# Kernel tuning notes

Hardware: AMD Instinct MI355X
Metric: run time of the kernel (lower is better)

Reference implementation:

```python
import jax, jax.numpy as jnp
import numpy as np

DIM = 256
HEAD_DIM = 64
NH = DIM // HEAD_DIM
PS = 2  # fine patch size
EPS = 1e-5


def _conv(x, w, b, stride, pad):
    y = jax.lax.conv_general_dilated(x, w, (stride, stride), ((pad, pad), (pad, pad)),
                                     dimension_numbers=('NCHW', 'OIHW', 'NCHW'))
    return y + b[None, :, None, None]


def _bn(x, g, b, m, v):
    s = g * jax.lax.rsqrt(v + EPS)
    return x * s[None, :, None, None] + (b - m * s)[None, :, None, None]


def setup_inputs() -> dict:
    key = jax.random.key(0)
    ks = jax.random.split(key, 24)
    C = DIM
    d = {}
    d['x'] = jax.random.normal(ks[0], (8, C, 64, 64), jnp.float32)
    # Downsample conv (C->C, k=4, s=2, p=1), torch OIHW layout
    d['w_down'] = jax.random.normal(ks[1], (C, C, 4, 4), jnp.float32) * 0.02
    d['b_down'] = jax.random.normal(ks[2], (C,), jnp.float32) * 0.02
    # coarse to_qkv Linear(64 -> 192), stored as [in, out]
    d['w_qkv_c'] = jax.random.normal(ks[3], (HEAD_DIM, 3 * HEAD_DIM), jnp.float32) * 0.05
    d['b_qkv_c'] = jax.random.normal(ks[4], (3 * HEAD_DIM,), jnp.float32) * 0.02
    # Upsample ConvTranspose2d (torch [in, out, kH, kW] layout)
    d['w_up'] = jax.random.normal(ks[5], (C, C, 4, 4), jnp.float32) * 0.02
    d['b_up'] = jax.random.normal(ks[6], (C,), jnp.float32) * 0.02
    # fine to_qkv Linear(64 -> 192)
    d['w_qkv_f'] = jax.random.normal(ks[7], (HEAD_DIM, 3 * HEAD_DIM), jnp.float32) * 0.05
    d['b_qkv_f'] = jax.random.normal(ks[8], (3 * HEAD_DIM,), jnp.float32) * 0.02
    # DWConv: depthwise 3x3 (groups=C) -> BN -> relu6 -> pointwise 1x1 -> BN -> relu6
    d['w_dw'] = jax.random.normal(ks[9], (C, 1, 3, 3), jnp.float32) * 0.1
    d['bn_dw_g'] = jax.random.uniform(ks[10], (C,), jnp.float32) * 0.5 + 0.75
    d['bn_dw_b'] = jax.random.normal(ks[11], (C,), jnp.float32) * 0.1
    d['bn_dw_m'] = jax.random.normal(ks[12], (C,), jnp.float32) * 0.1
    d['bn_dw_v'] = jax.random.uniform(ks[13], (C,), jnp.float32) + 0.5
    d['w_pw'] = jax.random.normal(ks[14], (C, C, 1, 1), jnp.float32) * 0.05
    d['bn_pw_g'] = jax.random.uniform(ks[15], (C,), jnp.float32) * 0.5 + 0.75
    d['bn_pw_b'] = jax.random.normal(ks[16], (C,), jnp.float32) * 0.1
    d['bn_pw_m'] = jax.random.normal(ks[17], (C,), jnp.float32) * 0.1
    d['bn_pw_v'] = jax.random.uniform(ks[18], (C,), jnp.float32) + 0.5
    return d


def reference(x, w_down, b_down, w_qkv_c, b_qkv_c, w_up, b_up, w_qkv_f, b_qkv_f,
              w_dw, bn_dw_g, bn_dw_b, bn_dw_m, bn_dw_v,
              w_pw, bn_pw_g, bn_pw_b, bn_pw_m, bn_pw_v):
    B, C, H, W = x.shape
    nh, hd = C // HEAD_DIM, HEAD_DIM
    scale = hd ** -0.5

    # ---- CoarseSelfAttention ----
    xd = _conv(x, w_down, b_down, 2, 1)           # [B,C,h,w]
    h, w = xd.shape[2], xd.shape[3]
    P = h * w
    tok = xd.reshape(B, nh, hd, P).transpose(0, 1, 3, 2)   # [B,nh,P,hd]
    q, k, v = jnp.split(tok @ w_qkv_c + b_qkv_c, 3, axis=-1)
    attn = jax.nn.softmax(jnp.einsum('bhqd,bhkd->bhqk', q, k) * scale, axis=-1)
    coarse_score = attn.sum(axis=-2)               # [B,nh,P]
    kf = max(1, P // 4)
    top_k = jax.lax.top_k(coarse_score, kf)[1]     # [B,nh,kf]
    out = jnp.einsum('bhqk,bhkd->bhqd', attn, v)
    out = out.transpose(0, 1, 3, 2).reshape(B, C, h, w)
    # ConvTranspose2d(k=4,s=2,p=1) as lhs-dilated conv with flipped/transposed kernel
    wt = jnp.flip(w_up, (2, 3)).transpose(1, 0, 2, 3)
    coarse = jax.lax.conv_general_dilated(out, wt, (1, 1), ((2, 2), (2, 2)),
                                          lhs_dilation=(2, 2),
                                          dimension_numbers=('NCHW', 'OIHW', 'NCHW'))
    coarse = coarse + b_up[None, :, None, None]
    # F.interpolate to (H,W) is identity here: upsample exactly restores HxW

    # ---- TopkSelfAttention ----
    ph, pw = H // PS, W // PS                      # ph*pw == P
    xh = coarse.reshape(B, nh, hd, ph, PS, pw, PS)
    patches = xh.transpose(0, 1, 2, 3, 5, 4, 6).reshape(B, nh, hd, ph * pw, PS, PS)
    idx = jnp.broadcast_to(top_k[:, :, None, :, None, None], (B, nh, hd, kf, PS, PS))
    sel = jnp.take_along_axis(patches, idx, axis=3)        # [B,nh,hd,kf,PS,PS]
    tokf = sel.reshape(B, nh, hd, kf, PS * PS).transpose(0, 1, 3, 4, 2)
    tokf = tokf.reshape(B, nh, kf * PS * PS, hd)
    qf, kk, vf = jnp.split(tokf @ w_qkv_f + b_qkv_f, 3, axis=-1)
    attnf = jax.nn.softmax(jnp.einsum('bhqd,bhkd->bhqk', qf, kk) * scale, axis=-1)
    outf = jnp.einsum('bhqk,bhkd->bhqd', attnf, vf)
    outf = outf.reshape(B, nh, kf, PS * PS, hd).transpose(0, 1, 2, 4, 3)
    outf = outf.reshape(B, nh, kf, hd, PS, PS)     # [B,nh,kf,hd,PS,PS]
    # scatter selected patches back into zeros (topk indices are unique per b,h)
    res = jnp.zeros((B, nh, ph * pw, hd, PS, PS), x.dtype)
    bi = jnp.arange(B)[:, None, None]
    hi = jnp.arange(nh)[None, :, None]
    res = res.at[bi, hi, top_k].set(outf)
    res = res.transpose(0, 1, 3, 2, 4, 5).reshape(B, nh, hd, ph, pw, PS, PS)
    region = res.transpose(0, 1, 2, 3, 5, 4, 6).reshape(B, C, H, W)

    y = coarse + region

    # ---- DWConv feed-forward ----
    yd = jax.lax.conv_general_dilated(y, w_dw, (1, 1), ((1, 1), (1, 1)),
                                      feature_group_count=C,
                                      dimension_numbers=('NCHW', 'OIHW', 'NCHW'))
    yd = jnp.clip(_bn(yd, bn_dw_g, bn_dw_b, bn_dw_m, bn_dw_v), 0.0, 6.0)
    yp = jax.lax.conv_general_dilated(yd, w_pw, (1, 1), ((0, 0), (0, 0)),
                                      dimension_numbers=('NCHW', 'OIHW', 'NCHW'))
    yp = jnp.clip(_bn(yp, bn_pw_g, bn_pw_b, bn_pw_m, bn_pw_v), 0.0, 6.0)
    return yp
```

## Files before the change

### kernel.cpp

```cpp
#include <hip/hip_runtime.h>
#include <cstdint>
#include <cstddef>


#define EPS_ 1e-5f

typedef short bf16x8_t __attribute__((ext_vector_type(8)));
typedef float f32x4_t __attribute__((ext_vector_type(4)));
#define MFMA16(a, b, c) __builtin_amdgcn_mfma_f32_16x16x32_bf16(a, b, c, 0, 0, 0)

__device__ __forceinline__ void cvt1(float f, unsigned short& h, unsigned short& l) {
  unsigned u = __float_as_uint(f);
  unsigned r = u + 0x7FFFu + ((u >> 16) & 1u);
  h = (unsigned short)(r >> 16);
  float lo = f - __uint_as_float(r & 0xFFFF0000u);
  l = (unsigned short)(__float_as_uint(lo) >> 16);
}
__device__ __forceinline__ void cvt2(float f0, float f1, unsigned& hpack, unsigned& lpack) {
  unsigned u0 = __float_as_uint(f0), u1 = __float_as_uint(f1);
  unsigned r0 = u0 + 0x7FFFu + ((u0 >> 16) & 1u);
  unsigned r1 = u1 + 0x7FFFu + ((u1 >> 16) & 1u);
  hpack = (r0 >> 16) | (r1 & 0xFFFF0000u);
  float l0 = f0 - __uint_as_float(r0 & 0xFFFF0000u);
  float l1 = f1 - __uint_as_float(r1 & 0xFFFF0000u);
  lpack = (__float_as_uint(l0) >> 16) | (__float_as_uint(l1) & 0xFFFF0000u);
}

__global__ __launch_bounds__(256) void k_pad_x(
    const float* __restrict__ x, float* __restrict__ xp) {
  const int plane = blockIdx.x;
  const float* src = x + (size_t)plane * 4096;
  float* dst = xp + (size_t)plane * 4356;
  for (int e = threadIdx.x; e < 4356; e += 256) {
    int r = e / 66, cc = e - r * 66;
    float v = 0.f;
    if (r >= 1 && r <= 64 && cc >= 1 && cc <= 64) v = src[(r - 1) * 64 + (cc - 1)];
    dst[e] = v;
  }
}

__global__ __launch_bounds__(256) void k_cvt_wdown(
    const float* __restrict__ w, unsigned short* __restrict__ wh,
    unsigned short* __restrict__ wl) {
  int e = blockIdx.x * 256 + threadIdx.x;
  cvt1(w[e], wh[e], wl[e]);
}

__global__ __launch_bounds__(256) void k_cvt_wqkv(
    const float* __restrict__ wq, unsigned short* __restrict__ wh,
    unsigned short* __restrict__ wl) {
  int e = blockIdx.x * 256 + threadIdx.x;
  int col = e >> 6, d = e & 63;
  float f = wq[d * 192 + col];
  if (col < 64) f *= 0.125f;
  cvt1(f, wh[e], wl[e]);
}

__global__ __launch_bounds__(256) void k_cvt_wup(
    const float* __restrict__ w_up, unsigned short* __restrict__ wth,
    unsigned short* __restrict__ wtl) {
  int e = blockIdx.x * 256 + threadIdx.x;
  int kp = e & 1023, oc = (e >> 10) & 255, c = e >> 18;
  int tap = kp >> 8, ic = kp & 255;
  int tk = tap >> 1, txi = tap & 1;
  int ry = c >> 1, rx = c & 1;
  int ky = (1 - ry) + 2 * tk, kx = (1 - rx) + 2 * txi;
  cvt1(w_up[((size_t)(ic * 256 + oc) * 4 + ky) * 4 + kx], wth[e], wtl[e]);
}

__global__ __launch_bounds__(256) void k_cvt_wpw(
    const float* __restrict__ w, unsigned short* __restrict__ wh,
    unsigned short* __restrict__ wl) {
  int e = blockIdx.x * 256 + threadIdx.x;
  cvt1(w[e], wh[e], wl[e]);
}

__device__ __forceinline__ void mfma_chunk(
    const unsigned short (*Ah)[72], const unsigned short (*Al)[72],
    const unsigned short (*Bh)[72], const unsigned short (*Bl)[72],
    f32x4_t (&acc)[4], int wm, int lane) {
  const int l16 = lane & 15, quad = lane >> 4;
#pragma unroll
  for (int ks = 0; ks < 2; ++ks) {
    int ko = ks * 32 + quad * 8;
    bf16x8_t ah = *(const bf16x8_t*)&Ah[wm + l16][ko];
    bf16x8_t al = *(const bf16x8_t*)&Al[wm + l16][ko];
#pragma unroll
    for (int nt = 0; nt < 4; ++nt) {
      bf16x8_t bh = *(const bf16x8_t*)&Bh[nt * 16 + l16][ko];
      bf16x8_t bl = *(const bf16x8_t*)&Bl[nt * 16 + l16][ko];
      acc[nt] = MFMA16(ah, bh, acc[nt]);
      acc[nt] = MFMA16(ah, bl, acc[nt]);
      acc[nt] = MFMA16(al, bh, acc[nt]);
    }
  }
}

__global__ __launch_bounds__(256) void k_conv_down_mfma(
    const float* __restrict__ xp, const unsigned short* __restrict__ wdh,
    const unsigned short* __restrict__ wdl, float* __restrict__ xd) {
  __shared__ unsigned short Ah[64][72], Al[64][72], Bh[64][72], Bl[64][72];
  const int t = threadIdx.x;
  const int pix0 = blockIdx.x * 64, oc0 = blockIdx.y * 64;
  const int bimg = pix0 >> 10, pos = pix0 & 1023;
  const int pl = t & 63, icg = t >> 6;
  const int rem = (pix0 + pl) & 1023;
  const int oy = rem >> 5, ox = rem & 31;
  const float* xb = xp + ((size_t)bimg * 256 + icg) * 4356 + (oy * 2) * 66 + ox * 2;
  const int wave = t >> 6, lane = t & 63, l16 = lane & 15, quad = lane >> 4;
  const int ar = t >> 3, akc = (t & 7) * 8;
  f32x4_t acc[4] = {};
  for (int kb = 0; kb < 4096; kb += 64) {
    bf16x8_t a0h = *(const bf16x8_t*)(wdh + (size_t)(oc0 + ar) * 4096 + kb + akc);
    bf16x8_t a0l = *(const bf16x8_t*)(wdl + (size_t)(oc0 + ar) * 4096 + kb + akc);
    bf16x8_t a1h = *(const bf16x8_t*)(wdh + (size_t)(oc0 + 32 + ar) * 4096 + kb + akc);
    bf16x8_t a1l = *(const bf16x8_t*)(wdl + (size_t)(oc0 + 32 + ar) * 4096 + kb + akc);
    float fv[16];
#pragma unroll
    for (int tap = 0; tap < 16; ++tap) fv[tap] = xb[(tap >> 2) * 66 + (tap & 3)];
    unsigned hp[8], lp[8];
#pragma unroll
    for (int j = 0; j < 8; ++j) cvt2(fv[2 * j], fv[2 * j + 1], hp[j], lp[j]);
    __syncthreads();
    *(bf16x8_t*)&Ah[ar][akc] = a0h;      *(bf16x8_t*)&Al[ar][akc] = a0l;
    *(bf16x8_t*)&Ah[ar + 32][akc] = a1h; *(bf16x8_t*)&Al[ar + 32][akc] = a1l;
    *(uint4*)&Bh[pl][icg * 16] = make_uint4(hp[0], hp[1], hp[2], hp[3]);
    *(uint4*)&Bh[pl][icg * 16 + 8] = make_uint4(hp[4], hp[5], hp[6], hp[7]);
    *(uint4*)&Bl[pl][icg * 16] = make_uint4(lp[0], lp[1], lp[2], lp[3]);
    *(uint4*)&Bl[pl][icg * 16 + 8] = make_uint4(lp[4], lp[5], lp[6], lp[7]);
    __syncthreads();
    mfma_chunk(Ah, Al, Bh, Bl, acc, wave * 16, lane);
    xb += 4 * 4356;
  }
#pragma unroll
  for (int r = 0; r < 4; ++r) {
    int oc = oc0 + wave * 16 + quad * 4 + r;
#pragma unroll
    for (int nt = 0; nt < 4; ++nt)
      xd[((size_t)(bimg * 256 + oc)) * 1024 + pos + nt * 16 + l16] = acc[nt][r];
  }
}

template <int MODE>
__global__ __launch_bounds__(256) void k_qkv_mfma(
    const float* __restrict__ src, const float* __restrict__ cbias,
    const unsigned short* __restrict__ wh, const unsigned short* __restrict__ wl,
    const float* __restrict__ bq, const int* __restrict__ topk,
    unsigned short* __restrict__ qh, unsigned short* __restrict__ ql,
    unsigned short* __restrict__ kh, unsigned short* __restrict__ kl,
    unsigned short* __restrict__ vth, unsigned short* __restrict__ vtl) {
  __shared__ unsigned short Ah[64][72], Al[64][72];
  const int t = threadIdx.x;
  const int tok0 = blockIdx.x * 64;
  const int pair = blockIdx.y;
  const int b = pair >> 2, h = pair & 3;
  const int tokl = t & 63, dg = t >> 6;
  float fv[16];
  if (MODE == 0) {
    const float* base = src + ((size_t)(b * 256 + h * 64 + dg * 16)) * 1024 + tok0 + tokl;
    const float* cb = cbias + h * 64 + dg * 16;
#pragma unroll
    for (int j = 0; j < 16; ++j) fv[j] = base[(size_t)j * 1024] + cb[j];
  } else {
    int tok = tok0 + tokl;
    int pp = topk[pair * 256 + (tok >> 2)];
    int py = (tok >> 1) & 1, px = tok & 1;
    int ry = (pp >> 5) * 2 + py, rx = (pp & 31) * 2 + px;
    const float* base = src + ((size_t)(b * 256 + h * 64 + dg * 16)) * 4096 + ry * 64 + rx;
#pragma unroll
    for (int j = 0; j < 16; ++j) fv[j] = base[(size_t)j * 4096];
  }
  unsigned hp[8], lp[8];
#pragma unroll
  for (int j = 0; j < 8; ++j) cvt2(fv[2 * j], fv[2 * j + 1], hp[j], lp[j]);
  *(uint4*)&Ah[tokl][dg * 16] = make_uint4(hp[0], hp[1], hp[2], hp[3]);
  *(uint4*)&Ah[tokl][dg * 16 + 8] = make_uint4(hp[4], hp[5], hp[6], hp[7]);
  *(uint4*)&Al[tokl][dg * 16] = make_uint4(lp[0], lp[1], lp[2], lp[3]);
  *(uint4*)&Al[tokl][dg * 16 + 8] = make_uint4(lp[4], lp[5], lp[6], lp[7]);
  __syncthreads();
  const int wave = t >> 6, lane = t & 63, l16 = lane & 15, quad = lane >> 4;
  f32x4_t acc[4][3] = {};
#pragma unroll
  for (int ks = 0; ks < 2; ++ks) {
    int ko = ks * 32 + quad * 8;
    bf16x8_t bh0[3], bl0[3];
#pragma unroll
    for (int nt = 0; nt < 3; ++nt) {
      int col = wave * 48 + nt * 16 + l16;
      bh0[nt] = *(const bf16x8_t*)(wh + col * 64 + ko);
      bl0[nt] = *(const bf16x8_t*)(wl + col * 64 + ko);
    }
#pragma unroll
    for (int mt = 0; mt < 4; ++mt) {
      bf16x8_t ah = *(const bf16x8_t*)&Ah[mt * 16 + l16][ko];
      bf16x8_t al = *(const bf16x8_t*)&Al[mt * 16 + l16][ko];
#pragma unroll
      for (int nt = 0; nt < 3; ++nt) {
        acc[mt][nt] = MFMA16(ah, bh0[nt], acc[mt][nt]);
        acc[mt][nt] = MFMA16(ah, bl0[nt], acc[mt][nt]);
        acc[mt][nt] = MFMA16(al, bh0[nt], acc[mt][nt]);
      }
    }
  }
#pragma unroll
  for (int nt = 0; nt < 3; ++nt) {
    int col = wave * 48 + nt * 16 + l16;
    float bqv = bq[col];
    if (col < 64) bqv *= 0.125f;
#pragma unroll
    for (int mt = 0; mt < 4; ++mt) {
#pragma unroll
      for (int r = 0; r < 4; ++r) {
        int tok = tok0 + mt * 16 + quad * 4 + r;
        float val = acc[mt][nt][r] + bqv;
        unsigned short hh, ll;
        cvt1(val, hh, ll);
        if (col < 64) {
          size_t o = ((size_t)pair * 1024 + tok) * 64 + col;
          qh[o] = hh; ql[o] = ll;
        } else if (col < 128) {
          size_t o = ((size_t)pair * 1024 + tok) * 64 + (col - 64);
          kh[o] = hh; kl[o] = ll;
        } else {
          size_t o = ((size_t)pair * 64 + (col - 128)) * 1024 + tok;
          vth[o] = hh; vtl[o] = ll;
        }
      }
    }
  }
}

template <int COARSE>
__global__ __launch_bounds__(256) void k_attn(
    const unsigned short* __restrict__ qh, const unsigned short* __restrict__ ql,
    const unsigned short* __restrict__ kh, const unsigned short* __restrict__ kl,
    const unsigned short* __restrict__ vth, const unsigned short* __restrict__ vtl,
    float* __restrict__ score, float* __restrict__ out) {
  __shared__ __align__(16) unsigned short Qb[2][64][72];
  __shared__ __align__(16) unsigned short Kb[2][64][72];
  __shared__ __align__(16) unsigned short Pb[2][64][72];
  __shared__ float mlW[4][2][64];
  __shared__ float mC[64], lC[64];
  __shared__ float colsum[1024];
  const int t = threadIdx.x;
  const int q0 = blockIdx.x * 64;
  const int pair = blockIdx.y;
  const int wave = t >> 6, lane = t & 63;
  const int l16 = lane & 15, quad = lane >> 4;
  const int wm = wave * 16;
  const int sr = t >> 3, skc = (t & 7) * 8;

  const size_t qbase = ((size_t)pair * 1024 + q0) * 64;
#pragma unroll
  for (int i = 0; i < 2; ++i) {
    int r = sr + i * 32;
    *(bf16x8_t*)&Qb[0][r][skc] = *(const bf16x8_t*)(qh + qbase + (size_t)r * 64 + skc);
    *(bf16x8_t*)&Qb[1][r][skc] = *(const bf16x8_t*)(ql + qbase + (size_t)r * 64 + skc);
  }
  if (COARSE) {
#pragma unroll
    for (int i = 0; i < 4; ++i) colsum[t + i * 256] = 0.f;
  }

  const size_t kmbase = (size_t)pair * 1024 * 64;
  const size_t vbase = (size_t)pair * 64 * 1024;

  float mrun[4] = {-1e30f, -1e30f, -1e30f, -1e30f};
  float lrun[4] = {0.f, 0.f, 0.f, 0.f};
  for (int kb = 0; kb < 1024; kb += 64) {
    __syncthreads();
#pragma unroll
    for (int i = 0; i < 2; ++i) {
      int r = sr + i * 32;
      *(bf16x8_t*)&Kb[0][r][skc] = *(const bf16x8_t*)(kh + kmbase + (size_t)(kb + r) * 64 + skc);
      *(bf16x8_t*)&Kb[1][r][skc] = *(const bf16x8_t*)(kl + kmbase + (size_t)(kb + r) * 64 + skc);
    }
    __syncthreads();
    f32x4_t acc[4] = {};
    mfma_chunk(Kb[0], Kb[1], Qb[0], Qb[1], acc, wm, lane);
#pragma unroll
    for (int nt = 0; nt < 4; ++nt) {
      float m0 = fmaxf(fmaxf(acc[nt][0], acc[nt][1]), fmaxf(acc[nt][2], acc[nt][3]));
      m0 = fmaxf(m0, __shfl_xor(m0, 16));
      m0 = fmaxf(m0, __shfl_xor(m0, 32));
      float mn = fmaxf(mrun[nt], m0);
      float s0 = __expf(acc[nt][0] - mn) + __expf(acc[nt][1] - mn) +
                 __expf(acc[nt][2] - mn) + __expf(acc[nt][3] - mn);
      s0 += __shfl_xor(s0, 16);
      s0 += __shfl_xor(s0, 32);
      lrun[nt] = lrun[nt] * __expf(mrun[nt] - mn) + s0;
      mrun[nt] = mn;
    }
  }
  __syncthreads();
  if (quad == 0) {
#pragma unroll
    for (int nt = 0; nt < 4; ++nt) {
      mlW[wave][0][nt * 16 + l16] = mrun[nt];
      mlW[wave][1][nt * 16 + l16] = lrun[nt];
    }
  }
  __syncthreads();
  if (t < 64) {
    float m0 = mlW[0][0][t], m1 = mlW[1][0][t], m2 = mlW[2][0][t], m3 = mlW[3][0][t];
    float mm = fmaxf(fmaxf(m0, m1), fmaxf(m2, m3));
    float ll = mlW[0][1][t] * __expf(m0 - mm) + mlW[1][1][t] * __expf(m1 - mm) +
               mlW[2][1][t] * __expf(m2 - mm) + mlW[3][1][t] * __expf(m3 - mm);
    mC[t] = mm;
    lC[t] = 1.0f / ll;
  }
  __syncthreads();
  float mq[4], il[4];
#pragma unroll
  for (int nt = 0; nt < 4; ++nt) {
    mq[nt] = mC[nt * 16 + l16];
    il[nt] = lC[nt * 16 + l16];
  }

  f32x4_t accO[4] = {};
  for (int kb = 0; kb < 1024; kb += 64) {
    __syncthreads();
#pragma unroll
    for (int i = 0; i < 2; ++i) {
      int r = sr + i * 32;
      *(bf16x8_t*)&Kb[0][r][skc] = *(const bf16x8_t*)(kh + kmbase + (size_t)(kb + r) * 64 + skc);
      *(bf16x8_t*)&Kb[1][r][skc] = *(const bf16x8_t*)(kl + kmbase + (size_t)(kb + r) * 64 + skc);
    }
    __syncthreads();
    f32x4_t acc[4] = {};
    mfma_chunk(Kb[0], Kb[1], Qb[0], Qb[1], acc, wm, lane);
    float P[4][4];
#pragma unroll
    for (int nt = 0; nt < 4; ++nt)
#pragma unroll
      for (int r = 0; r < 4; ++r) P[nt][r] = __expf(acc[nt][r] - mq[nt]) * il[nt];
    if (COARSE) {
#pragma unroll
      for (int r = 0; r < 4; ++r) {
        float cs = P[0][r] + P[1][r] + P[2][r] + P[3][r];
        cs += __shfl_xor(cs, 1);
        cs += __shfl_xor(cs, 2);
        cs += __shfl_xor(cs, 4);
        cs += __shfl_xor(cs, 8);
        if (l16 == 0) colsum[kb + wm + quad * 4 + r] += cs;
      }
    }
    __syncthreads();
#pragma unroll
    for (int nt = 0; nt < 4; ++nt) {
      unsigned h01, l01, h23, l23;
      cvt2(P[nt][0], P[nt][1], h01, l01);
      cvt2(P[nt][2], P[nt][3], h23, l23);
      *(uint2*)&Pb[0][nt * 16 + l16][wm + quad * 4] = make_uint2(h01, h23);
      *(uint2*)&Pb[1][nt * 16 + l16][wm + quad * 4] = make_uint2(l01, l23);
    }
#pragma unroll
    for (int i = 0; i < 2; ++i) {
      int r = sr + i * 32;
      *(bf16x8_t*)&Kb[0][r][skc] = *(const bf16x8_t*)(vth + vbase + (size_t)r * 1024 + kb + skc);
      *(bf16x8_t*)&Kb[1][r][skc] = *(const bf16x8_t*)(vtl + vbase + (size_t)r * 1024 + kb + skc);
    }
    __syncthreads();
    mfma_chunk(Pb[0], Pb[1], Kb[0], Kb[1], accO, wm, lane);
  }
  __syncthreads();

  if (COARSE) {
#pragma unroll
    for (int i = 0; i < 4; ++i)
      atomicAdd(&score[pair * 1024 + t + i * 256], colsum[t + i * 256]);
    float (*Tr)[68] = reinterpret_cast<float(*)[68]>(&Pb[0][0][0]);
#pragma unroll
    for (int nt = 0; nt < 4; ++nt)
#pragma unroll
      for (int r = 0; r < 4; ++r)
        Tr[nt * 16 + l16][wm + quad * 4 + r] = accO[nt][r];
    __syncthreads();
    const int b = pair >> 2, h = pair & 3;
#pragma unroll
    for (int i = 0; i < 16; ++i) {
      int e = t + i * 256;
      int d = e >> 6, ql_ = e & 63;
      int pix = q0 + ql_;
      int iy = (pix >> 5) + 1, ix = (pix & 31) + 1;
      out[((size_t)(b * 256 + h * 64 + d)) * 1156 + iy * 34 + ix] = Tr[d][ql_];
    }
  } else {
#pragma unroll
    for (int nt = 0; nt < 4; ++nt)
#pragma unroll
      for (int r = 0; r < 4; ++r) {
        int qm = q0 + wm + quad * 4 + r;
        out[((size_t)pair * 1024 + qm) * 64 + nt * 16 + l16] = accO[nt][r];
      }
  }
}

__global__ __launch_bounds__(256) void k_topk(
    const float* __restrict__ score, int* __restrict__ idx) {
  __shared__ unsigned long long key[1024];
  const int pair = blockIdx.x;
  const int t = threadIdx.x;
#pragma unroll
  for (int j = 0; j < 4; ++j) {
    int i = t + j * 256;
    unsigned u = __float_as_uint(score[pair * 1024 + i]);
    u = u ^ ((u & 0x80000000u) ? 0xFFFFFFFFu : 0x80000000u);
    u = ~u;
    key[i] = ((unsigned long long)u << 32) | (unsigned)i;
  }
  __syncthreads();
  for (int k = 2; k <= 1024; k <<= 1) {
    for (int j = k >> 1; j > 0; j >>= 1) {
      for (int w = 0; w < 4; ++w) {
        int i = t + w * 256;
        int l = i ^ j;
        if (l > i) {
          bool up = ((i & k) == 0);
          unsigned long long a = key[i], b = key[l];
          if ((a > b) == up) { key[i] = b; key[l] = a; }
        }
      }
      __syncthreads();
    }
  }
  idx[pair * 256 + t] = (int)(key[t] & 0xFFFFFFFFu);
}

__global__ __launch_bounds__(256) void k_convT_mfma(
    const float* __restrict__ inp, const unsigned short* __restrict__ wth,
    const unsigned short* __restrict__ wtl, const float* __restrict__ bias,
    float* __restrict__ out) {
  __shared__ unsigned short Ah[64][72], Al[64][72], Bh[64][72], Bl[64][72];
  const int t = threadIdx.x;
  const int pix0 = blockIdx.x * 64;
  const int oc0 = blockIdx.y * 64;
  const int cls = blockIdx.z;
  const int ry = cls >> 1, rx = cls & 1;
  const int b = pix0 >> 10;
  const int wave = t >> 6, lane = t & 63;
  const int l16 = lane & 15, quad = lane >> 4;
  const int pixl = t & 63, icg = t >> 6;
  const int remg = (pix0 + pixl) & 1023;
  const int tyy = remg >> 5, txx = remg & 31;
  f32x4_t acc[4] = {};
  const size_t wbase = ((size_t)cls * 256 + oc0) * 1024;
  for (int kb = 0; kb < 1024; kb += 64) {
    const int tap = kb >> 8, ic0 = kb & 255;
    const int tk = tap >> 1, txi = tap & 1;
    const int iy = tyy + ry + 1 - tk, ix = txx + rx + 1 - txi;
    const float* p = inp + (size_t)(b * 256 + ic0 + icg * 16) * 1156 + iy * 34 + ix;
    float fv[16];
#pragma unroll
    for (int j = 0; j < 16; ++j) fv[j] = p[(size_t)j * 1156];
    unsigned hp[8], lpk[8];
#pragma unroll
    for (int j = 0; j < 8; ++j) cvt2(fv[2 * j], fv[2 * j + 1], hp[j], lpk[j]);
    bf16x8_t a0h, a0l, a1h, a1l;
    {
      int r = t >> 3, kc = (t & 7) * 8;
      a0h = *(const bf16x8_t*)(wth + wbase + (size_t)r * 1024 + kb + kc);
      a0l = *(const bf16x8_t*)(wtl + wbase + (size_t)r * 1024 + kb + kc);
      a1h = *(const bf16x8_t*)(wth + wbase + (size_t)(r + 32) * 1024 + kb + kc);
      a1l = *(const bf16x8_t*)(wtl + wbase + (size_t)(r + 32) * 1024 + kb + kc);
    }
    __syncthreads();
    {
      int r = t >> 3, kc = (t & 7) * 8;
      *(bf16x8_t*)&Ah[r][kc] = a0h;      *(bf16x8_t*)&Al[r][kc] = a0l;
      *(bf16x8_t*)&Ah[r + 32][kc] = a1h; *(bf16x8_t*)&Al[r + 32][kc] = a1l;
    }
    *(uint4*)&Bh[pixl][icg * 16] = make_uint4(hp[0], hp[1], hp[2], hp[3]);
    *(uint4*)&Bh[pixl][icg * 16 + 8] = make_uint4(hp[4], hp[5], hp[6], hp[7]);
    *(uint4*)&Bl[pixl][icg * 16] = make_uint4(lpk[0], lpk[1], lpk[2], lpk[3]);
    *(uint4*)&Bl[pixl][icg * 16 + 8] = make_uint4(lpk[4], lpk[5], lpk[6], lpk[7]);
    __syncthreads();
    mfma_chunk(Ah, Al, Bh, Bl, acc, wave * 16, lane);
  }
  __syncthreads();
#pragma unroll
  for (int r = 0; r < 4; ++r) {
    int oc = oc0 + wave * 16 + quad * 4 + r;
    float bvs = bias[oc];
#pragma unroll
    for (int nt = 0; nt < 4; ++nt) {
      int pix = pix0 + nt * 16 + l16;
      int rem2 = pix & 1023;
      int y = (rem2 >> 5) * 2 + ry, xx = (rem2 & 31) * 2 + rx;
      out[((size_t)(b * 256 + oc) * 64 + y) * 64 + xx] = acc[nt][r] + bvs;
    }
  }
}

__global__ __launch_bounds__(256) void k_scatter(
    const float* __restrict__ outf, const int* __restrict__ idx,
    float* __restrict__ y) {
  int g = blockIdx.x * 256 + threadIdx.x;
  int pair = g >> 16;
  int rem = g & 65535;
  int tok = rem >> 6, d = rem & 63;
  int b = pair >> 2, h = pair & 3;
  int pp = idx[pair * 256 + (tok >> 2)];
  int py = (tok >> 1) & 1, px = tok & 1;
  int ry = (pp >> 5) * 2 + py, rx = (pp & 31) * 2 + px;
  y[((size_t)(b * 256 + h * 64 + d) * 64 + ry) * 64 + rx] += outf[g];
}

__global__ __launch_bounds__(256) void k_dwconv(
    const float* __restrict__ y, const float* __restrict__ wdw,
    const float* __restrict__ g, const float* __restrict__ bb,
    const float* __restrict__ m, const float* __restrict__ vv,
    float* __restrict__ yd) {
  int gi = blockIdx.x * 256 + threadIdx.x;
  int x = gi & 63, yy = (gi >> 6) & 63, ch = (gi >> 12) & 255, b = gi >> 20;
  const float* plane = y + (size_t)(b * 256 + ch) * 4096;
  const float* wc = wdw + ch * 9;
  float s = 0.f;
#pragma unroll
  for (int ky = 0; ky < 3; ++ky) {
    int iy = yy + ky - 1;
    if (iy < 0 || iy >= 64) continue;
#pragma unroll
    for (int kx = 0; kx < 3; ++kx) {
      int ix = x + kx - 1;
      if (ix < 0 || ix >= 64) continue;
      s = fmaf(plane[iy * 64 + ix], wc[ky * 3 + kx], s);
    }
  }
  float sc = g[ch] * rsqrtf(vv[ch] + EPS_);
  float val = s * sc + (bb[ch] - m[ch] * sc);
  yd[gi] = fminf(fmaxf(val, 0.f), 6.f);
}

__global__ __launch_bounds__(256) void k_pw_mfma(
    const float* __restrict__ yd, const unsigned short* __restrict__ wh,
    const unsigned short* __restrict__ wl, const float* __restrict__ g,
    const float* __restrict__ bb, const float* __restrict__ m,
    const float* __restrict__ vv, float* __restrict__ out) {
  __shared__ unsigned short Ah[64][72], Al[64][72], Bh[64][72], Bl[64][72];
  const int t = threadIdx.x;
  const int pix0 = blockIdx.x * 64;
  const int oc0 = blockIdx.y * 64;
  const int b = pix0 >> 12, pos0 = pix0 & 4095;
  const int wave = t >> 6, lane = t & 63;
  const int l16 = lane & 15, quad = lane >> 4;
  const int pixl = t & 63, icg = t >> 6;
  f32x4_t acc[4] = {};
  for (int kb = 0; kb < 256; kb += 64) {
    float fv[16];
#pragma unroll
    for (int j = 0; j < 16; ++j)
      fv[j] = yd[(size_t)(b * 256 + kb + icg * 16 + j) * 4096 + pos0 + pixl];
    unsigned hp[8], lpk[8];
#pragma unroll
    for (int j = 0; j < 8; ++j) cvt2(fv[2 * j], fv[2 * j + 1], hp[j], lpk[j]);
    bf16x8_t a0h, a0l, a1h, a1l;
    {
      int r = t >> 3, kc = (t & 7) * 8;
      a0h = *(const bf16x8_t*)(wh + (size_t)(oc0 + r) * 256 + kb + kc);
      a0l = *(const bf16x8_t*)(wl + (size_t)(oc0 + r) * 256 + kb + kc);
      a1h = *(const bf16x8_t*)(wh + (size_t)(oc0 + r + 32) * 256 + kb + kc);
      a1l = *(const bf16x8_t*)(wl + (size_t)(oc0 + r + 32) * 256 + kb + kc);
    }
    __syncthreads();
    {
      int r = t >> 3, kc = (t & 7) * 8;
      *(bf16x8_t*)&Ah[r][kc] = a0h;      *(bf16x8_t*)&Al[r][kc] = a0l;
      *(bf16x8_t*)&Ah[r + 32][kc] = a1h; *(bf16x8_t*)&Al[r + 32][kc] = a1l;
    }
    *(uint4*)&Bh[pixl][icg * 16] = make_uint4(hp[0], hp[1], hp[2], hp[3]);
    *(uint4*)&Bh[pixl][icg * 16 + 8] = make_uint4(hp[4], hp[5], hp[6], hp[7]);
    *(uint4*)&Bl[pixl][icg * 16] = make_uint4(lpk[0], lpk[1], lpk[2], lpk[3]);
    *(uint4*)&Bl[pixl][icg * 16 + 8] = make_uint4(lpk[4], lpk[5], lpk[6], lpk[7]);
    __syncthreads();
    mfma_chunk(Ah, Al, Bh, Bl, acc, wave * 16, lane);
    __syncthreads();
  }
#pragma unroll
  for (int r = 0; r < 4; ++r) {
    int oc = oc0 + wave * 16 + quad * 4 + r;
    float sc = g[oc] * rsqrtf(vv[oc] + EPS_);
    float off = bb[oc] - m[oc] * sc;
#pragma unroll
    for (int nt = 0; nt < 4; ++nt) {
      int pix = pos0 + nt * 16 + l16;
      float val = fminf(fmaxf(acc[nt][r] * sc + off, 0.f), 6.f);
      out[(size_t)(b * 256 + oc) * 4096 + pix] = val;
    }
  }
}

extern "C" void kernel_launch(void* const* d_in, const int* in_sizes, int n_in,
                              void* d_out, int out_size, void* d_ws, size_t ws_size,
                              hipStream_t stream) {
  (void)in_sizes; (void)n_in; (void)out_size; (void)ws_size;
  const float* x       = (const float*)d_in[0];
  const float* w_down  = (const float*)d_in[1];
  const float* b_down  = (const float*)d_in[2];
  const float* w_qkv_c = (const float*)d_in[3];
  const float* b_qkv_c = (const float*)d_in[4];
  const float* w_up    = (const float*)d_in[5];
  const float* b_up    = (const float*)d_in[6];
  const float* w_qkv_f = (const float*)d_in[7];
  const float* b_qkv_f = (const float*)d_in[8];
  const float* w_dw    = (const float*)d_in[9];
  const float* bn_dw_g = (const float*)d_in[10];
  const float* bn_dw_b = (const float*)d_in[11];
  const float* bn_dw_m = (const float*)d_in[12];
  const float* bn_dw_v = (const float*)d_in[13];
  const float* w_pw    = (const float*)d_in[14];
  const float* bn_pw_g = (const float*)d_in[15];
  const float* bn_pw_b = (const float*)d_in[16];
  const float* bn_pw_m = (const float*)d_in[17];
  const float* bn_pw_v = (const float*)d_in[18];

  float* ws = (float*)d_ws;
  float*          scratch= ws;
  unsigned short* qh     = (unsigned short*)(ws + 33554432);
  unsigned short* ql     = (unsigned short*)(ws + 34603008);
  unsigned short* kh     = (unsigned short*)(ws + 35651584);
  unsigned short* kl     = (unsigned short*)(ws + 36700160);
  unsigned short* vth    = (unsigned short*)(ws + 37748736);
  unsigned short* vtl    = (unsigned short*)(ws + 38797312);
  float*          xd     = ws + 39845888;
  float*          outcp  = ws + 41943040;
  float*          coarse = ws + 44310528;
  float*          outf   = ws + 52699136;
  float*          score  = ws + 54796288;
  unsigned short* wdh    = (unsigned short*)(ws + 54829056);
  unsigned short* wdl    = (unsigned short*)(ws + 55353344);
  unsigned short* wt_hi  = (unsigned short*)(ws + 55877632);
  unsigned short* wt_lo  = (unsigned short*)(ws + 56401920);
  unsigned short* wpw_hi = (unsigned short*)(ws + 56926208);
  unsigned short* wpw_lo = (unsigned short*)(ws + 56958976);
  unsigned short* wqh_c  = (unsigned short*)(ws + 56991744);
  unsigned short* wql_c  = (unsigned short*)(ws + 56997888);
  unsigned short* wqh_f  = (unsigned short*)(ws + 57004032);
  unsigned short* wql_f  = (unsigned short*)(ws + 57010176);
  int*            idx    = (int*)(ws + 57016320);
  float*          xp     = scratch;
  float*          yd     = scratch;

  hipMemsetAsync(score, 0, 32768 * sizeof(float), stream);
  hipMemsetAsync(outcp, 0, (size_t)2367488 * sizeof(float), stream);
  k_pad_x<<<2048, 256, 0, stream>>>(x, xp);
  k_cvt_wdown<<<4096, 256, 0, stream>>>(w_down, wdh, wdl);
  k_cvt_wqkv<<<48, 256, 0, stream>>>(w_qkv_c, wqh_c, wql_c);
  k_cvt_wqkv<<<48, 256, 0, stream>>>(w_qkv_f, wqh_f, wql_f);
  k_cvt_wup<<<4096, 256, 0, stream>>>(w_up, wt_hi, wt_lo);
  k_cvt_wpw<<<256, 256, 0, stream>>>(w_pw, wpw_hi, wpw_lo);

  k_conv_down_mfma<<<dim3(128, 4), 256, 0, stream>>>(xp, wdh, wdl, xd);
  k_qkv_mfma<0><<<dim3(16, 32), 256, 0, stream>>>(xd, b_down, wqh_c, wql_c, b_qkv_c,
                                                  nullptr, qh, ql, kh, kl, vth, vtl);
  k_attn<1><<<dim3(16, 32), 256, 0, stream>>>(qh, ql, kh, kl, vth, vtl, score, outcp);
  k_topk<<<32, 256, 0, stream>>>(score, idx);
  k_convT_mfma<<<dim3(128, 4, 4), 256, 0, stream>>>(outcp, wt_hi, wt_lo, b_up, coarse);

  k_qkv_mfma<1><<<dim3(16, 32), 256, 0, stream>>>(coarse, nullptr, wqh_f, wql_f, b_qkv_f,
                                                  idx, qh, ql, kh, kl, vth, vtl);
  k_attn<0><<<dim3(16, 32), 256, 0, stream>>>(qh, ql, kh, kl, vth, vtl, nullptr, outf);
  k_scatter<<<8192, 256, 0, stream>>>(outf, idx, coarse);
  k_dwconv<<<32768, 256, 0, stream>>>(coarse, w_dw, bn_dw_g, bn_dw_b, bn_dw_m, bn_dw_v, yd);
  k_pw_mfma<<<dim3(512, 4), 256, 0, stream>>>(yd, wpw_hi, wpw_lo, bn_pw_g, bn_pw_b,
                                              bn_pw_m, bn_pw_v, (float*)d_out);
}
```

Baseline: 638.4 us.

## Store intermediate activations pre-split into packed bf16 hi/lo pairs

```diff
diff --git a/kernel.cpp b/kernel.cpp
--- a/kernel.cpp
+++ b/kernel.cpp
@@ -15,6 +15,11 @@
   h = (unsigned short)(r >> 16);
   float lo = f - __uint_as_float(r & 0xFFFF0000u);
   l = (unsigned short)(__float_as_uint(lo) >> 16);
+}
+__device__ __forceinline__ unsigned cvtpack(float f) {
+  unsigned short h, l;
+  cvt1(f, h, l);
+  return (unsigned)h | ((unsigned)l << 16);
 }
 __device__ __forceinline__ void cvt2(float f0, float f1, unsigned& hpack, unsigned& lpack) {
   unsigned u0 = __float_as_uint(f0), u1 = __float_as_uint(f1);
@@ -25,17 +30,23 @@
   float l1 = f1 - __uint_as_float(r1 & 0xFFFF0000u);
   lpack = (__float_as_uint(l0) >> 16) | (__float_as_uint(l1) & 0xFFFF0000u);
 }
+__device__ __forceinline__ unsigned pk_h(unsigned a, unsigned b) {
+  return (a & 0xFFFFu) | (b << 16);
+}
+__device__ __forceinline__ unsigned pk_l(unsigned a, unsigned b) {
+  return (a >> 16) | (b & 0xFFFF0000u);
+}
 
 __global__ __launch_bounds__(256) void k_pad_x(
-    const float* __restrict__ x, float* __restrict__ xp) {
+    const float* __restrict__ x, unsigned* __restrict__ xphl) {
   const int plane = blockIdx.x;
   const float* src = x + (size_t)plane * 4096;
-  float* dst = xp + (size_t)plane * 4356;
+  unsigned* dst = xphl + (size_t)plane * 4488;
   for (int e = threadIdx.x; e < 4356; e += 256) {
     int r = e / 66, cc = e - r * 66;
     float v = 0.f;
     if (r >= 1 && r <= 64 && cc >= 1 && cc <= 64) v = src[(r - 1) * 64 + (cc - 1)];
-    dst[e] = v;
+    dst[r * 68 + cc] = cvtpack(v);
   }
 }
 
@@ -97,8 +108,9 @@
 }
 
 __global__ __launch_bounds__(256) void k_conv_down_mfma(
-    const float* __restrict__ xp, const unsigned short* __restrict__ wdh,
-    const unsigned short* __restrict__ wdl, float* __restrict__ xd) {
+    const unsigned* __restrict__ xphl, const unsigned short* __restrict__ wdh,
+    const unsigned short* __restrict__ wdl, const float* __restrict__ bias,
+    unsigned* __restrict__ xdhl) {
   __shared__ unsigned short Ah[64][72], Al[64][72], Bh[64][72], Bl[64][72];
   const int t = threadIdx.x;
   const int pix0 = blockIdx.x * 64, oc0 = blockIdx.y * 64;
@@ -106,7 +118,7 @@
   const int pl = t & 63, icg = t >> 6;
   const int rem = (pix0 + pl) & 1023;
   const int oy = rem >> 5, ox = rem & 31;
-  const float* xb = xp + ((size_t)bimg * 256 + icg) * 4356 + (oy * 2) * 66 + ox * 2;
+  const unsigned* xb = xphl + ((size_t)bimg * 256 + icg) * 4488 + (oy * 2) * 68 + ox * 2;
   const int wave = t >> 6, lane = t & 63, l16 = lane & 15, quad = lane >> 4;
   const int ar = t >> 3, akc = (t & 7) * 8;
   f32x4_t acc[4] = {};
@@ -115,35 +127,39 @@
     bf16x8_t a0l = *(const bf16x8_t*)(wdl + (size_t)(oc0 + ar) * 4096 + kb + akc);
     bf16x8_t a1h = *(const bf16x8_t*)(wdh + (size_t)(oc0 + 32 + ar) * 4096 + kb + akc);
     bf16x8_t a1l = *(const bf16x8_t*)(wdl + (size_t)(oc0 + 32 + ar) * 4096 + kb + akc);
-    float fv[16];
-#pragma unroll
-    for (int tap = 0; tap < 16; ++tap) fv[tap] = xb[(tap >> 2) * 66 + (tap & 3)];
-    unsigned hp[8], lp[8];
-#pragma unroll
-    for (int j = 0; j < 8; ++j) cvt2(fv[2 * j], fv[2 * j + 1], hp[j], lp[j]);
+    unsigned hA[8], lA[8];
+#pragma unroll
+    for (int r = 0; r < 4; ++r) {
+      uint2 u01 = *(const uint2*)(xb + r * 68);
+      uint2 u23 = *(const uint2*)(xb + r * 68 + 2);
+      hA[2 * r] = pk_h(u01.x, u01.y); hA[2 * r + 1] = pk_h(u23.x, u23.y);
+      lA[2 * r] = pk_l(u01.x, u01.y); lA[2 * r + 1] = pk_l(u23.x, u23.y);
+    }
     __syncthreads();
     *(bf16x8_t*)&Ah[ar][akc] = a0h;      *(bf16x8_t*)&Al[ar][akc] = a0l;
     *(bf16x8_t*)&Ah[ar + 32][akc] = a1h; *(bf16x8_t*)&Al[ar + 32][akc] = a1l;
-    *(uint4*)&Bh[pl][icg * 16] = make_uint4(hp[0], hp[1], hp[2], hp[3]);
-    *(uint4*)&Bh[pl][icg * 16 + 8] = make_uint4(hp[4], hp[5], hp[6], hp[7]);
-    *(uint4*)&Bl[pl][icg * 16] = make_uint4(lp[0], lp[1], lp[2], lp[3]);
-    *(uint4*)&Bl[pl][icg * 16 + 8] = make_uint4(lp[4], lp[5], lp[6], lp[7]);
+    *(uint4*)&Bh[pl][icg * 16] = make_uint4(hA[0], hA[1], hA[2], hA[3]);
+    *(uint4*)&Bh[pl][icg * 16 + 8] = make_uint4(hA[4], hA[5], hA[6], hA[7]);
+    *(uint4*)&Bl[pl][icg * 16] = make_uint4(lA[0], lA[1], lA[2], lA[3]);
+    *(uint4*)&Bl[pl][icg * 16 + 8] = make_uint4(lA[4], lA[5], lA[6], lA[7]);
     __syncthreads();
     mfma_chunk(Ah, Al, Bh, Bl, acc, wave * 16, lane);
-    xb += 4 * 4356;
+    xb += 4 * 4488;
   }
 #pragma unroll
   for (int r = 0; r < 4; ++r) {
     int oc = oc0 + wave * 16 + quad * 4 + r;
+    float bv = bias[oc];
 #pragma unroll
     for (int nt = 0; nt < 4; ++nt)
-      xd[((size_t)(bimg * 256 + oc)) * 1024 + pos + nt * 16 + l16] = acc[nt][r];
+      xdhl[((size_t)(bimg * 256 + oc)) * 1024 + pos + nt * 16 + l16] =
+          cvtpack(acc[nt][r] + bv);
   }
 }
 
 template <int MODE>
 __global__ __launch_bounds__(256) void k_qkv_mfma(
-    const float* __restrict__ src, const float* __restrict__ cbias,
+    const unsigned* __restrict__ srcp, const float* __restrict__ srcf,
     const unsigned short* __restrict__ wh, const unsigned short* __restrict__ wl,
     const float* __restrict__ bq, const int* __restrict__ topk,
     unsigned short* __restrict__ qh, unsigned short* __restrict__ ql,
@@ -155,24 +171,29 @@
   const int pair = blockIdx.y;
   const int b = pair >> 2, h = pair & 3;
   const int tokl = t & 63, dg = t >> 6;
-  float fv[16];
+  unsigned hp[8], lp[8];
   if (MODE == 0) {
-    const float* base = src + ((size_t)(b * 256 + h * 64 + dg * 16)) * 1024 + tok0 + tokl;
-    const float* cb = cbias + h * 64 + dg * 16;
-#pragma unroll
-    for (int j = 0; j < 16; ++j) fv[j] = base[(size_t)j * 1024] + cb[j];
+    const unsigned* base = srcp + ((size_t)(b * 256 + h * 64 + dg * 16)) * 1024 + tok0 + tokl;
+    unsigned u[16];
+#pragma unroll
+    for (int j = 0; j < 16; ++j) u[j] = base[(size_t)j * 1024];
+#pragma unroll
+    for (int j = 0; j < 8; ++j) {
+      hp[j] = pk_h(u[2 * j], u[2 * j + 1]);
+      lp[j] = pk_l(u[2 * j], u[2 * j + 1]);
+    }
   } else {
     int tok = tok0 + tokl;
     int pp = topk[pair * 256 + (tok >> 2)];
     int py = (tok >> 1) & 1, px = tok & 1;
     int ry = (pp >> 5) * 2 + py, rx = (pp & 31) * 2 + px;
-    const float* base = src + ((size_t)(b * 256 + h * 64 + dg * 16)) * 4096 + ry * 64 + rx;
+    const float* base = srcf + ((size_t)(b * 256 + h * 64 + dg * 16)) * 4096 + ry * 64 + rx;
+    float fv[16];
 #pragma unroll
     for (int j = 0; j < 16; ++j) fv[j] = base[(size_t)j * 4096];
-  }
-  unsigned hp[8], lp[8];
-#pragma unroll
-  for (int j = 0; j < 8; ++j) cvt2(fv[2 * j], fv[2 * j + 1], hp[j], lp[j]);
+#pragma unroll
+    for (int j = 0; j < 8; ++j) cvt2(fv[2 * j], fv[2 * j + 1], hp[j], lp[j]);
+  }
   *(uint4*)&Ah[tokl][dg * 16] = make_uint4(hp[0], hp[1], hp[2], hp[3]);
   *(uint4*)&Ah[tokl][dg * 16 + 8] = make_uint4(hp[4], hp[5], hp[6], hp[7]);
   *(uint4*)&Al[tokl][dg * 16] = make_uint4(lp[0], lp[1], lp[2], lp[3]);
@@ -235,7 +256,8 @@
     const unsigned short* __restrict__ qh, const unsigned short* __restrict__ ql,
     const unsigned short* __restrict__ kh, const unsigned short* __restrict__ kl,
     const unsigned short* __restrict__ vth, const unsigned short* __restrict__ vtl,
-    float* __restrict__ score, float* __restrict__ out) {
+    float* __restrict__ score, unsigned* __restrict__ outc,
+    float* __restrict__ outf) {
   __shared__ __align__(16) unsigned short Qb[2][64][72];
   __shared__ __align__(16) unsigned short Kb[2][64][72];
   __shared__ __align__(16) unsigned short Pb[2][64][72];
@@ -383,7 +405,7 @@
       int d = e >> 6, ql_ = e & 63;
       int pix = q0 + ql_;
       int iy = (pix >> 5) + 1, ix = (pix & 31) + 1;
-      out[((size_t)(b * 256 + h * 64 + d)) * 1156 + iy * 34 + ix] = Tr[d][ql_];
+      outc[((size_t)(b * 256 + h * 64 + d)) * 1156 + iy * 34 + ix] = cvtpack(Tr[d][ql_]);
     }
   } else {
 #pragma unroll
@@ -391,7 +413,7 @@
 #pragma unroll
       for (int r = 0; r < 4; ++r) {
         int qm = q0 + wm + quad * 4 + r;
-        out[((size_t)pair * 1024 + qm) * 64 + nt * 16 + l16] = accO[nt][r];
+        outf[((size_t)pair * 1024 + qm) * 64 + nt * 16 + l16] = accO[nt][r];
       }
   }
 }
@@ -428,7 +450,7 @@
 }
 
 __global__ __launch_bounds__(256) void k_convT_mfma(
-    const float* __restrict__ inp, const unsigned short* __restrict__ wth,
+    const unsigned* __restrict__ inp, const unsigned short* __restrict__ wth,
     const unsigned short* __restrict__ wtl, const float* __restrict__ bias,
     float* __restrict__ out) {
   __shared__ unsigned short Ah[64][72], Al[64][72], Bh[64][72], Bl[64][72];
@@ -449,13 +471,16 @@
     const int tap = kb >> 8, ic0 = kb & 255;
     const int tk = tap >> 1, txi = tap & 1;
     const int iy = tyy + ry + 1 - tk, ix = txx + rx + 1 - txi;
-    const float* p = inp + (size_t)(b * 256 + ic0 + icg * 16) * 1156 + iy * 34 + ix;
-    float fv[16];
-#pragma unroll
-    for (int j = 0; j < 16; ++j) fv[j] = p[(size_t)j * 1156];
+    const unsigned* p = inp + (size_t)(b * 256 + ic0 + icg * 16) * 1156 + iy * 34 + ix;
+    unsigned u[16];
+#pragma unroll
+    for (int j = 0; j < 16; ++j) u[j] = p[(size_t)j * 1156];
     unsigned hp[8], lpk[8];
 #pragma unroll
-    for (int j = 0; j < 8; ++j) cvt2(fv[2 * j], fv[2 * j + 1], hp[j], lpk[j]);
+    for (int j = 0; j < 8; ++j) {
+      hp[j] = pk_h(u[2 * j], u[2 * j + 1]);
+      lpk[j] = pk_l(u[2 * j], u[2 * j + 1]);
+    }
     bf16x8_t a0h, a0l, a1h, a1l;
     {
       int r = t >> 3, kc = (t & 7) * 8;
@@ -510,7 +535,7 @@
     const float* __restrict__ y, const float* __restrict__ wdw,
     const float* __restrict__ g, const float* __restrict__ bb,
     const float* __restrict__ m, const float* __restrict__ vv,
-    float* __restrict__ yd) {
+    unsigned* __restrict__ ydhl) {
   int gi = blockIdx.x * 256 + threadIdx.x;
   int x = gi & 63, yy = (gi >> 6) & 63, ch = (gi >> 12) & 255, b = gi >> 20;
   const float* plane = y + (size_t)(b * 256 + ch) * 4096;
@@ -529,11 +554,11 @@
   }
   float sc = g[ch] * rsqrtf(vv[ch] + EPS_);
   float val = s * sc + (bb[ch] - m[ch] * sc);
-  yd[gi] = fminf(fmaxf(val, 0.f), 6.f);
+  ydhl[gi] = cvtpack(fminf(fmaxf(val, 0.f), 6.f));
 }
 
 __global__ __launch_bounds__(256) void k_pw_mfma(
-    const float* __restrict__ yd, const unsigned short* __restrict__ wh,
+    const unsigned* __restrict__ ydhl, const unsigned short* __restrict__ wh,
     const unsigned short* __restrict__ wl, const float* __restrict__ g,
     const float* __restrict__ bb, const float* __restrict__ m,
     const float* __restrict__ vv, float* __restrict__ out) {
@@ -547,13 +572,16 @@
   const int pixl = t & 63, icg = t >> 6;
   f32x4_t acc[4] = {};
   for (int kb = 0; kb < 256; kb += 64) {
-    float fv[16];
+    unsigned u[16];
 #pragma unroll
     for (int j = 0; j < 16; ++j)
-      fv[j] = yd[(size_t)(b * 256 + kb + icg * 16 + j) * 4096 + pos0 + pixl];
+      u[j] = ydhl[(size_t)(b * 256 + kb + icg * 16 + j) * 4096 + pos0 + pixl];
     unsigned hp[8], lpk[8];
 #pragma unroll
-    for (int j = 0; j < 8; ++j) cvt2(fv[2 * j], fv[2 * j + 1], hp[j], lpk[j]);
+    for (int j = 0; j < 8; ++j) {
+      hp[j] = pk_h(u[2 * j], u[2 * j + 1]);
+      lpk[j] = pk_l(u[2 * j], u[2 * j + 1]);
+    }
     bf16x8_t a0h, a0l, a1h, a1l;
     {
       int r = t >> 3, kc = (t & 7) * 8;
@@ -615,15 +643,16 @@
   const float* bn_pw_v = (const float*)d_in[18];
 
   float* ws = (float*)d_ws;
-  float*          scratch= ws;
+  unsigned*       xphl   = (unsigned*)ws;
+  unsigned*       ydhl   = (unsigned*)ws;
   unsigned short* qh     = (unsigned short*)(ws + 33554432);
   unsigned short* ql     = (unsigned short*)(ws + 34603008);
   unsigned short* kh     = (unsigned short*)(ws + 35651584);
   unsigned short* kl     = (unsigned short*)(ws + 36700160);
   unsigned short* vth    = (unsigned short*)(ws + 37748736);
   unsigned short* vtl    = (unsigned short*)(ws + 38797312);
-  float*          xd     = ws + 39845888;
-  float*          outcp  = ws + 41943040;
+  unsigned*       xdhl   = (unsigned*)(ws + 39845888);
+  unsigned*       outcphl= (unsigned*)(ws + 41943040);
   float*          coarse = ws + 44310528;
   float*          outf   = ws + 52699136;
   float*          score  = ws + 54796288;
@@ -638,30 +667,30 @@
   unsigned short* wqh_f  = (unsigned short*)(ws + 57004032);
   unsigned short* wql_f  = (unsigned short*)(ws + 57010176);
   int*            idx    = (int*)(ws + 57016320);
-  float*          xp     = scratch;
-  float*          yd     = scratch;
 
   hipMemsetAsync(score, 0, 32768 * sizeof(float), stream);
-  hipMemsetAsync(outcp, 0, (size_t)2367488 * sizeof(float), stream);
-  k_pad_x<<<2048, 256, 0, stream>>>(x, xp);
+  hipMemsetAsync(outcphl, 0, (size_t)2367488 * sizeof(unsigned), stream);
+  k_pad_x<<<2048, 256, 0, stream>>>(x, xphl);
   k_cvt_wdown<<<4096, 256, 0, stream>>>(w_down, wdh, wdl);
   k_cvt_wqkv<<<48, 256, 0, stream>>>(w_qkv_c, wqh_c, wql_c);
   k_cvt_wqkv<<<48, 256, 0, stream>>>(w_qkv_f, wqh_f, wql_f);
   k_cvt_wup<<<4096, 256, 0, stream>>>(w_up, wt_hi, wt_lo);
   k_cvt_wpw<<<256, 256, 0, stream>>>(w_pw, wpw_hi, wpw_lo);
 
-  k_conv_down_mfma<<<dim3(128, 4), 256, 0, stream>>>(xp, wdh, wdl, xd);
-  k_qkv_mfma<0><<<dim3(16, 32), 256, 0, stream>>>(xd, b_down, wqh_c, wql_c, b_qkv_c,
+  k_conv_down_mfma<<<dim3(128, 4), 256, 0, stream>>>(xphl, wdh, wdl, b_down, xdhl);
+  k_qkv_mfma<0><<<dim3(16, 32), 256, 0, stream>>>(xdhl, nullptr, wqh_c, wql_c, b_qkv_c,
                                                   nullptr, qh, ql, kh, kl, vth, vtl);
-  k_attn<1><<<dim3(16, 32), 256, 0, stream>>>(qh, ql, kh, kl, vth, vtl, score, outcp);
+  k_attn<1><<<dim3(16, 32), 256, 0, stream>>>(qh, ql, kh, kl, vth, vtl, score,
+                                              outcphl, nullptr);
   k_topk<<<32, 256, 0, stream>>>(score, idx);
-  k_convT_mfma<<<dim3(128, 4, 4), 256, 0, stream>>>(outcp, wt_hi, wt_lo, b_up, coarse);
-
-  k_qkv_mfma<1><<<dim3(16, 32), 256, 0, stream>>>(coarse, nullptr, wqh_f, wql_f, b_qkv_f,
+  k_convT_mfma<<<dim3(128, 4, 4), 256, 0, stream>>>(outcphl, wt_hi, wt_lo, b_up, coarse);
+
+  k_qkv_mfma<1><<<dim3(16, 32), 256, 0, stream>>>(nullptr, coarse, wqh_f, wql_f, b_qkv_f,
                                                   idx, qh, ql, kh, kl, vth, vtl);
-  k_attn<0><<<dim3(16, 32), 256, 0, stream>>>(qh, ql, kh, kl, vth, vtl, nullptr, outf);
+  k_attn<0><<<dim3(16, 32), 256, 0, stream>>>(qh, ql, kh, kl, vth, vtl, nullptr,
+                                              nullptr, outf);
   k_scatter<<<8192, 256, 0, stream>>>(outf, idx, coarse);
-  k_dwconv<<<32768, 256, 0, stream>>>(coarse, w_dw, bn_dw_g, bn_dw_b, bn_dw_m, bn_dw_v, yd);
-  k_pw_mfma<<<dim3(512, 4), 256, 0, stream>>>(yd, wpw_hi, wpw_lo, bn_pw_g, bn_pw_b,
+  k_dwconv<<<32768, 256, 0, stream>>>(coarse, w_dw, bn_dw_g, bn_dw_b, bn_dw_m, bn_dw_v, ydhl);
+  k_pw_mfma<<<dim3(512, 4), 256, 0, stream>>>(ydhl, wpw_hi, wpw_lo, bn_pw_g, bn_pw_b,
                                               bn_pw_m, bn_pw_v, (float*)d_out);
 }
```

Measured after the change: 627.4 us. Within noise of the previous version (-1.7%).
